# Kernel optimization log

Hardware: AMD Instinct MI355X
Metric: run time of the kernel (lower is better)

## Reference

```python
import jax, jax.numpy as jnp
import numpy as np

B, D, FH, FW, C = 8, 41, 32, 88, 64
OGFH, OGFW = 512, 1408
DX = jnp.array([0.5, 20.0, 0.5], dtype=jnp.float32)          # voxel sizes (x, y, z)
BX = jnp.array([-49.75, 0.0, -49.75], dtype=jnp.float32)    # voxel centers origin
NX = (200, 1, 200)                                           # grid dims (x, y, z)
NSEG = NX[0] * NX[1] * NX[2] * B                             # 320000 voxel-batch slots


def _frustum():
    # (D, FH, FW, 3) pixel-u, pixel-v, depth; matches create_frustum_1camera
    ds = jnp.broadcast_to(jnp.arange(4.0, 45.0, 1.0)[:, None, None], (D, FH, FW))
    xs = jnp.broadcast_to(jnp.linspace(0.0, OGFW - 1, FW)[None, None, :], (D, FH, FW))
    ys = jnp.broadcast_to(jnp.linspace(0.0, OGFH - 1, FH)[None, :, None], (D, FH, FW))
    return jnp.stack([xs, ys, ds], axis=-1).astype(jnp.float32)


def setup_inputs() -> dict:
    key = jax.random.key(0)
    k1, = jax.random.split(key, 1)
    x = jax.random.normal(k1, (B, D, FH, FW, C), dtype=jnp.float32)
    # realistic pinhole intrinsics: fx=fy=800, principal point at image center
    K = np.array([[800.0, 0.0, OGFW / 2.0],
                  [0.0, 800.0, OGFH / 2.0],
                  [0.0, 0.0, 1.0]], dtype=np.float32)
    intrins = jnp.asarray(np.broadcast_to(K, (B, 3, 3)).copy())
    post_rots = jnp.broadcast_to(jnp.eye(3, dtype=jnp.float32), (B, 3, 3)) + jnp.zeros((B, 3, 3), jnp.float32)
    post_trans = jnp.zeros((B, 3), dtype=jnp.float32)
    return {"x": x, "intrins": intrins, "post_rots": post_rots, "post_trans": post_trans}


def _forward(x, intrins, post_rots, post_trans):
    # ---- get_geometry ----
    pts = _frustum()[None] - post_trans[:, None, None, None, :]          # (B,D,FH,FW,3)
    pts = jnp.einsum('bij,bdhwj->bdhwi', jnp.linalg.inv(post_rots), pts)
    pts = jnp.concatenate([pts[..., :2] * pts[..., 2:3], pts[..., 2:3]], axis=-1)
    geom = jnp.einsum('bij,bdhwj->bdhwi', jnp.linalg.inv(intrins), pts)  # camera-frame xyz

    # ---- voxel_splat ----
    Nprime = B * D * FH * FW
    xf = x.reshape(Nprime, C)
    # torch .long() truncates toward zero -> float->int cast in jnp also truncates
    coords = ((geom - (BX - DX / 2.0)) / DX).reshape(Nprime, 3).astype(jnp.int32)
    batch_ix = jnp.repeat(jnp.arange(B, dtype=jnp.int32), Nprime // B)
    kept = ((coords[:, 0] >= 0) & (coords[:, 0] < NX[0]) &
            (coords[:, 1] >= 0) & (coords[:, 1] < NX[1]) &
            (coords[:, 2] >= 0) & (coords[:, 2] < NX[2]))
    ranks = (coords[:, 0] * (NX[1] * NX[2] * B) + coords[:, 1] * (NX[2] * B) +
             coords[:, 2] * B + batch_ix)
    ranks = jnp.where(kept, ranks, NSEG)  # dump out-of-grid points into extra segment
    # segment-sum == sort + cumsum-trick pooling (sum of features per voxel)
    pooled = jax.ops.segment_sum(xf, ranks, num_segments=NSEG + 1)[:-1]  # (NSEG, C)
    final = pooled.reshape(NX[0], NX[1], NX[2], B, C)       # rank order: (x, y, z, b)
    final = jnp.transpose(final, (3, 4, 1, 2, 0))            # (B, C, ny, nz, nx)
    # torch.cat(final.unbind(dim=2), 1) -> stack ny slices along channel dim
    out = jnp.transpose(final, (0, 2, 1, 3, 4)).reshape(B, NX[1] * C, NX[2], NX[0])
    return out


def reference(x, intrins, post_rots, post_trans):
    return _forward(x, intrins, post_rots, post_trans)
```

## Files before the change

kernel.cpp:

```cpp
#include <hip/hip_runtime.h>

#define BB 8
#define DD 41
#define FHH 32
#define FWW 88
#define CC 64
#define NXX 200
#define NXZ 200
#define PLANE (NXZ * NXX)
#define OUT_ELEMS (BB * CC * PLANE)
#define ROWP 204

__global__ __launch_bounds__(256) void lss_zero_prep(
        float* __restrict__ out,
        const float* __restrict__ intrins,
        const float* __restrict__ post_rots,
        float* __restrict__ ws) {
#pragma clang fp contract(off)
    if (blockIdx.x == 0 && threadIdx.x < BB) {
        int b = threadIdx.x;
        const float* mats[2] = { post_rots + b * 9, intrins + b * 9 };
        for (int m = 0; m < 2; ++m) {
            const float* a = mats[m];
            float* o = ws + b * 18 + m * 9;
            float c00 = a[4] * a[8] - a[5] * a[7];
            float c01 = a[5] * a[6] - a[3] * a[8];
            float c02 = a[3] * a[7] - a[4] * a[6];
            float det = a[0] * c00 + a[1] * c01 + a[2] * c02;
            o[0] = c00 / det;
            o[1] = (a[2] * a[7] - a[1] * a[8]) / det;
            o[2] = (a[1] * a[5] - a[2] * a[4]) / det;
            o[3] = c01 / det;
            o[4] = (a[0] * a[8] - a[2] * a[6]) / det;
            o[5] = (a[2] * a[3] - a[0] * a[5]) / det;
            o[6] = c02 / det;
            o[7] = (a[1] * a[6] - a[0] * a[7]) / det;
            o[8] = (a[0] * a[4] - a[1] * a[3]) / det;
        }
    }
    float4 z = make_float4(0.0f, 0.0f, 0.0f, 0.0f);
    float4* o4 = reinterpret_cast<float4*>(out);
    const int n4 = OUT_ELEMS / 4;
    for (int i = blockIdx.x * 256 + threadIdx.x; i < n4; i += gridDim.x * 256)
        o4[i] = z;
}

__global__ __launch_bounds__(512) void lss_splat(
        const float* __restrict__ x,
        const float* __restrict__ post_trans,
        const float* __restrict__ invmats,
        float* __restrict__ out) {
#pragma clang fp contract(off)
    __shared__ float    srow[CC * ROWP];
    __shared__ int      scx[FWW];
    __shared__ unsigned smask[FWW];
    __shared__ int      scz;

    int blk = blockIdx.x;
    int d = blk % DD;
    int b = blk / DD;
    int tid = threadIdx.x;

    for (int i = tid; i < CC * ROWP; i += 512) srow[i] = 0.0f;

    {
        const float stepx = 1407.0f / 87.0f;
        const float stepy = 511.0f / 31.0f;
        const float* iR = invmats + b * 18;
        const float* iK = iR + 9;
        float t0 = post_trans[b * 3 + 0];
        float t1 = post_trans[b * 3 + 1];
        float t2 = post_trans[b * 3 + 2];
        float dv = 4.0f + (float)d;

        for (int t = tid; t < FWW * FHH; t += 512) {
            int w = t >> 5;
            int h = t & 31;
            float u = (float)w * stepx;
            float v = (float)h * stepy;
            float q0 = u - t0, q1 = v - t1, q2 = dv - t2;
            float p0 = fmaf(iR[2], q2, fmaf(iR[1], q1, iR[0] * q0));
            float p1 = fmaf(iR[5], q2, fmaf(iR[4], q1, iR[3] * q0));
            float p2 = fmaf(iR[8], q2, fmaf(iR[7], q1, iR[6] * q0));
            float s0 = p0 * p2;
            float s1 = p1 * p2;
            float s2 = p2;
            float g0 = fmaf(iK[2], s2, fmaf(iK[1], s1, iK[0] * s0));
            float g1 = fmaf(iK[5], s2, fmaf(iK[4], s1, iK[3] * s0));
            float g2 = fmaf(iK[8], s2, fmaf(iK[7], s1, iK[6] * s0));
            float cxf = (g0 + 50.0f) * 2.0f;
            float cyf = (g1 + 10.0f) / 20.0f;
            float czf = (g2 + 50.0f) * 2.0f;
            int cx = (int)cxf;
            int cy = (int)cyf;
            int cz = (int)czf;
            bool kept = (cx >= 0) & (cx < NXX) & (cy == 0) & (cz >= 0) & (cz < NXZ);
            unsigned long long m = __ballot(kept);
            int lane = tid & 63;
            if (lane == 0) {
                smask[w] = (unsigned)m;
                scx[w]   = min(NXX - 1, max(0, cx));
            } else if (lane == 32) {
                smask[w] = (unsigned)(m >> 32);
                scx[w]   = min(NXX - 1, max(0, cx));
            }
            if (t == 0) scz = cz;
        }
    }
    __syncthreads();

    int wv   = tid >> 6;
    int lane = tid & 63;
    int wsub = lane >> 4;
    int cq   = lane & 15;

    for (int j = 0; j < 3; ++j) {
        int w0 = 4 * wv + 32 * j;
        if (w0 >= FWW) break;
        int w = w0 + wsub;

        unsigned m = smask[w];
        int cx = scx[w];
        const float* colp = x + (((size_t)(b * DD + d) * FHH) * FWW + w) * CC + cq * 4;

        float4 acc = make_float4(0.0f, 0.0f, 0.0f, 0.0f);
#pragma unroll
        for (int hb = 0; hb < 4; ++hb) {
            float4 vals[8];
#pragma unroll
            for (int k = 0; k < 8; ++k)
                vals[k] = *reinterpret_cast<const float4*>(
                    colp + (size_t)(hb * 8 + k) * (FWW * CC));
#pragma unroll
            for (int k = 0; k < 8; ++k) {
                bool bt = (m >> (hb * 8 + k)) & 1u;
                acc.x += bt ? vals[k].x : 0.0f;
                acc.y += bt ? vals[k].y : 0.0f;
                acc.z += bt ? vals[k].z : 0.0f;
                acc.w += bt ? vals[k].w : 0.0f;
            }
        }
        if (m) {
            atomicAdd(&srow[(cq * 4 + 0) * ROWP + cx], acc.x);
            atomicAdd(&srow[(cq * 4 + 1) * ROWP + cx], acc.y);
            atomicAdd(&srow[(cq * 4 + 2) * ROWP + cx], acc.z);
            atomicAdd(&srow[(cq * 4 + 3) * ROWP + cx], acc.w);
        }
    }
    __syncthreads();

    int cz = scz;
    if (cz >= 0 && cz < NXZ) {
        size_t outBase = ((size_t)b * CC) * PLANE + (size_t)cz * NXX;
        for (int i = tid; i < CC * NXX; i += 512) {
            int c   = i / NXX;
            int cxi = i - c * NXX;
            out[outBase + (size_t)c * PLANE + cxi] = srow[c * ROWP + cxi];
        }
    }
}

extern "C" void kernel_launch(void* const* d_in, const int* in_sizes, int n_in,
                              void* d_out, int out_size, void* d_ws, size_t ws_size,
                              hipStream_t stream) {
    const float* x          = (const float*)d_in[0];
    const float* intrins    = (const float*)d_in[1];
    const float* post_rots  = (const float*)d_in[2];
    const float* post_trans = (const float*)d_in[3];
    float* out = (float*)d_out;
    float* ws  = (float*)d_ws;

    lss_zero_prep<<<2048, 256, 0, stream>>>(out, intrins, post_rots, ws);
    lss_splat<<<BB * DD, 512, 0, stream>>>(x, post_trans, ws, out);
}
```

Before: 76.88 us.

## Split splat into per-width tiles with global atomics and selective row zeroing

The splat is re-partitioned from one block per (batch, depth) to one block per (batch, depth, 8-column group), so many more blocks can run concurrently. Per-column sums are reduced with wave shuffles and added straight to the output with global atomics, replacing the full shared-memory row buffer. Zeroing is now done per output row: a small pre-kernel clears the rows that some depth maps to, and extra blocks in the splat kernel clear only the rows no depth covers, so the full-output memset pass goes away. In exchange the output needs global atomics and every block recomputes the 3x3 inverses; correctness also depends on the covered rows being cleared before any atomics land.

```diff
diff --git a/kernel.cpp b/kernel.cpp
--- a/kernel.cpp
+++ b/kernel.cpp
@@ -8,154 +8,211 @@
 #define NXX 200
 #define NXZ 200
 #define PLANE (NXZ * NXX)
-#define OUT_ELEMS (BB * CC * PLANE)
-#define ROWP 204
-
-__global__ __launch_bounds__(256) void lss_zero_prep(
-        float* __restrict__ out,
-        const float* __restrict__ intrins,
-        const float* __restrict__ post_rots,
-        float* __restrict__ ws) {
-#pragma clang fp contract(off)
-    if (blockIdx.x == 0 && threadIdx.x < BB) {
-        int b = threadIdx.x;
-        const float* mats[2] = { post_rots + b * 9, intrins + b * 9 };
-        for (int m = 0; m < 2; ++m) {
-            const float* a = mats[m];
-            float* o = ws + b * 18 + m * 9;
-            float c00 = a[4] * a[8] - a[5] * a[7];
-            float c01 = a[5] * a[6] - a[3] * a[8];
-            float c02 = a[3] * a[7] - a[4] * a[6];
-            float det = a[0] * c00 + a[1] * c01 + a[2] * c02;
-            o[0] = c00 / det;
-            o[1] = (a[2] * a[7] - a[1] * a[8]) / det;
-            o[2] = (a[1] * a[5] - a[2] * a[4]) / det;
-            o[3] = c01 / det;
-            o[4] = (a[0] * a[8] - a[2] * a[6]) / det;
-            o[5] = (a[2] * a[3] - a[0] * a[5]) / det;
-            o[6] = c02 / det;
-            o[7] = (a[1] * a[6] - a[0] * a[7]) / det;
-            o[8] = (a[0] * a[4] - a[1] * a[3]) / det;
-        }
-    }
-    float4 z = make_float4(0.0f, 0.0f, 0.0f, 0.0f);
-    float4* o4 = reinterpret_cast<float4*>(out);
-    const int n4 = OUT_ELEMS / 4;
-    for (int i = blockIdx.x * 256 + threadIdx.x; i < n4; i += gridDim.x * 256)
-        o4[i] = z;
+#define WG 8
+#define NWG (FWW / WG)
+#define NTILE (BB * DD * NWG)
+#define NROWS (BB * NXZ)
+#define STEPX (1407.0f / 87.0f)
+#define STEPY (511.0f / 31.0f)
+
+__device__ __forceinline__ void inv3x3(const float* __restrict__ a, float* o) {
+#pragma clang fp contract(off)
+    float c00 = a[4] * a[8] - a[5] * a[7];
+    float c01 = a[5] * a[6] - a[3] * a[8];
+    float c02 = a[3] * a[7] - a[4] * a[6];
+    float det = a[0] * c00 + a[1] * c01 + a[2] * c02;
+    o[0] = c00 / det;
+    o[1] = (a[2] * a[7] - a[1] * a[8]) / det;
+    o[2] = (a[1] * a[5] - a[2] * a[4]) / det;
+    o[3] = c01 / det;
+    o[4] = (a[0] * a[8] - a[2] * a[6]) / det;
+    o[5] = (a[2] * a[3] - a[0] * a[5]) / det;
+    o[6] = c02 / det;
+    o[7] = (a[1] * a[6] - a[0] * a[7]) / det;
+    o[8] = (a[0] * a[4] - a[1] * a[3]) / det;
+}
+
+__device__ __forceinline__ int cz_of(const float* iR, const float* iK,
+                                     float t0, float t1, float t2, int d) {
+#pragma clang fp contract(off)
+    float dv = 4.0f + (float)d;
+    float q0 = 0.0f - t0, q1 = 0.0f - t1, q2 = dv - t2;
+    float p0 = fmaf(iR[2], q2, fmaf(iR[1], q1, iR[0] * q0));
+    float p1 = fmaf(iR[5], q2, fmaf(iR[4], q1, iR[3] * q0));
+    float p2 = fmaf(iR[8], q2, fmaf(iR[7], q1, iR[6] * q0));
+    float s0 = p0 * p2, s1 = p1 * p2, s2 = p2;
+    float g2 = fmaf(iK[8], s2, fmaf(iK[7], s1, iK[6] * s0));
+    float czf = (g2 + 50.0f) * 2.0f;
+    return (int)czf;
+}
+
+__global__ __launch_bounds__(256) void lss_zero_cov(
+        const float* __restrict__ intrins, const float* __restrict__ post_rots,
+        const float* __restrict__ post_trans, float* __restrict__ out) {
+#pragma clang fp contract(off)
+    __shared__ int scz;
+    int blk = blockIdx.x;
+    int d = blk % DD, b = blk / DD;
+    if (threadIdx.x == 0) {
+        float iR[9], iK[9];
+        inv3x3(post_rots + b * 9, iR);
+        inv3x3(intrins + b * 9, iK);
+        scz = cz_of(iR, iK, post_trans[b*3], post_trans[b*3+1], post_trans[b*3+2], d);
+    }
+    __syncthreads();
+    int cz = scz;
+    if (cz < 0 || cz >= NXZ) return;
+    float4 z = make_float4(0.f, 0.f, 0.f, 0.f);
+    size_t base = ((size_t)b * CC) * PLANE + (size_t)cz * NXX;
+    for (int i = threadIdx.x; i < CC * (NXX / 4); i += 256) {
+        int c = i / (NXX / 4), q = i - c * (NXX / 4);
+        *reinterpret_cast<float4*>(out + base + (size_t)c * PLANE + q * 4) = z;
+    }
 }
 
 __global__ __launch_bounds__(512) void lss_splat(
         const float* __restrict__ x,
-        const float* __restrict__ post_trans,
-        const float* __restrict__ invmats,
-        float* __restrict__ out) {
-#pragma clang fp contract(off)
-    __shared__ float    srow[CC * ROWP];
-    __shared__ int      scx[FWW];
-    __shared__ unsigned smask[FWW];
-    __shared__ int      scz;
+        const float* __restrict__ intrins, const float* __restrict__ post_rots,
+        const float* __restrict__ post_trans, float* __restrict__ out) {
+#pragma clang fp contract(off)
+    __shared__ float sInv[18];
+    __shared__ int   scx[WG];
+    __shared__ unsigned smask[WG];
+    __shared__ int   scz;
+    __shared__ float ltile[WG][CC + 1];
+    __shared__ int   sflag;
 
     int blk = blockIdx.x;
-    int d = blk % DD;
-    int b = blk / DD;
     int tid = threadIdx.x;
 
-    for (int i = tid; i < CC * ROWP; i += 512) srow[i] = 0.0f;
-
-    {
-        const float stepx = 1407.0f / 87.0f;
-        const float stepy = 511.0f / 31.0f;
-        const float* iR = invmats + b * 18;
-        const float* iK = iR + 9;
-        float t0 = post_trans[b * 3 + 0];
-        float t1 = post_trans[b * 3 + 1];
-        float t2 = post_trans[b * 3 + 2];
+    if (blk >= NTILE) {
+        int r  = blk - NTILE;
+        int b  = r / NXZ;
+        int czr = r - b * NXZ;
+        if (tid == 0) {
+            inv3x3(post_rots + b * 9, sInv);
+            inv3x3(intrins  + b * 9, sInv + 9);
+        }
+        __syncthreads();
+        if (tid < 64) {
+            bool cov = false;
+            if (tid < DD)
+                cov = (cz_of(sInv, sInv + 9, post_trans[b*3], post_trans[b*3+1],
+                             post_trans[b*3+2], tid) == czr);
+            int any = __any(cov);
+            if (tid == 0) sflag = any;
+        }
+        __syncthreads();
+        if (sflag) return;
+        float4 z = make_float4(0.f, 0.f, 0.f, 0.f);
+        size_t base = ((size_t)b * CC) * PLANE + (size_t)czr * NXX;
+        for (int i = tid; i < CC * (NXX / 4); i += 512) {
+            int c = i / (NXX / 4), q = i - c * (NXX / 4);
+            *reinterpret_cast<float4*>(out + base + (size_t)c * PLANE + q * 4) = z;
+        }
+        return;
+    }
+
+    int wg = blk % NWG;
+    int t2 = blk / NWG;
+    int d  = t2 % DD;
+    int b  = t2 / DD;
+    int w0 = wg * WG;
+
+    float t0 = post_trans[b * 3 + 0];
+    float t1 = post_trans[b * 3 + 1];
+    float t2f = post_trans[b * 3 + 2];
+
+    if (tid == 0) {
+        inv3x3(post_rots + b * 9, sInv);
+        inv3x3(intrins  + b * 9, sInv + 9);
+    }
+    __syncthreads();
+
+    if (tid < WG * FHH) {
+        int wi = tid >> 5;
+        int h  = tid & 31;
+        const float* iR = sInv;
+        const float* iK = sInv + 9;
+        float u  = (float)(w0 + wi) * STEPX;
+        float v  = (float)h * STEPY;
         float dv = 4.0f + (float)d;
-
-        for (int t = tid; t < FWW * FHH; t += 512) {
-            int w = t >> 5;
-            int h = t & 31;
-            float u = (float)w * stepx;
-            float v = (float)h * stepy;
-            float q0 = u - t0, q1 = v - t1, q2 = dv - t2;
-            float p0 = fmaf(iR[2], q2, fmaf(iR[1], q1, iR[0] * q0));
-            float p1 = fmaf(iR[5], q2, fmaf(iR[4], q1, iR[3] * q0));
-            float p2 = fmaf(iR[8], q2, fmaf(iR[7], q1, iR[6] * q0));
-            float s0 = p0 * p2;
-            float s1 = p1 * p2;
-            float s2 = p2;
-            float g0 = fmaf(iK[2], s2, fmaf(iK[1], s1, iK[0] * s0));
-            float g1 = fmaf(iK[5], s2, fmaf(iK[4], s1, iK[3] * s0));
-            float g2 = fmaf(iK[8], s2, fmaf(iK[7], s1, iK[6] * s0));
-            float cxf = (g0 + 50.0f) * 2.0f;
-            float cyf = (g1 + 10.0f) / 20.0f;
-            float czf = (g2 + 50.0f) * 2.0f;
-            int cx = (int)cxf;
-            int cy = (int)cyf;
-            int cz = (int)czf;
-            bool kept = (cx >= 0) & (cx < NXX) & (cy == 0) & (cz >= 0) & (cz < NXZ);
-            unsigned long long m = __ballot(kept);
-            int lane = tid & 63;
-            if (lane == 0) {
-                smask[w] = (unsigned)m;
-                scx[w]   = min(NXX - 1, max(0, cx));
-            } else if (lane == 32) {
-                smask[w] = (unsigned)(m >> 32);
-                scx[w]   = min(NXX - 1, max(0, cx));
-            }
-            if (t == 0) scz = cz;
-        }
+        float q0 = u - t0, q1 = v - t1, q2 = dv - t2f;
+        float p0 = fmaf(iR[2], q2, fmaf(iR[1], q1, iR[0] * q0));
+        float p1 = fmaf(iR[5], q2, fmaf(iR[4], q1, iR[3] * q0));
+        float p2 = fmaf(iR[8], q2, fmaf(iR[7], q1, iR[6] * q0));
+        float s0 = p0 * p2, s1 = p1 * p2, s2 = p2;
+        float g0 = fmaf(iK[2], s2, fmaf(iK[1], s1, iK[0] * s0));
+        float g1 = fmaf(iK[5], s2, fmaf(iK[4], s1, iK[3] * s0));
+        float g2 = fmaf(iK[8], s2, fmaf(iK[7], s1, iK[6] * s0));
+        float cxf = (g0 + 50.0f) * 2.0f;
+        float cyf = (g1 + 10.0f) / 20.0f;
+        float czf = (g2 + 50.0f) * 2.0f;
+        int cx = (int)cxf;
+        int cy = (int)cyf;
+        int cz = (int)czf;
+        bool kept = (cx >= 0) & (cx < NXX) & (cy == 0) & (cz >= 0) & (cz < NXZ);
+        unsigned long long m = __ballot(kept);
+        int lane = tid & 63;
+        if (lane == 0) {
+            smask[wi] = (unsigned)m;
+            scx[wi]   = min(NXX - 1, max(0, cx));
+        } else if (lane == 32) {
+            smask[wi] = (unsigned)(m >> 32);
+            scx[wi]   = min(NXX - 1, max(0, cx));
+        }
+        if (tid == 0)
+            scz = cz_of(iR, iK, t0, t1, t2f, d);
     }
     __syncthreads();
 
     int wv   = tid >> 6;
     int lane = tid & 63;
-    int wsub = lane >> 4;
     int cq   = lane & 15;
-
-    for (int j = 0; j < 3; ++j) {
-        int w0 = 4 * wv + 32 * j;
-        if (w0 >= FWW) break;
-        int w = w0 + wsub;
-
-        unsigned m = smask[w];
-        int cx = scx[w];
-        const float* colp = x + (((size_t)(b * DD + d) * FHH) * FWW + w) * CC + cq * 4;
-
-        float4 acc = make_float4(0.0f, 0.0f, 0.0f, 0.0f);
+    int hsub = lane >> 4;
+    int w    = w0 + wv;
+
+    const float* colp = x + (((size_t)(b * DD + d) * FHH) * FWW + w) * CC + cq * 4;
+    unsigned m = smask[wv];
+
+    float4 vals[8];
 #pragma unroll
-        for (int hb = 0; hb < 4; ++hb) {
-            float4 vals[8];
+    for (int hh = 0; hh < 8; ++hh) {
+        int h = hh * 4 + hsub;
+        vals[hh] = *reinterpret_cast<const float4*>(colp + (size_t)h * (FWW * CC));
+    }
+    float4 acc = make_float4(0.f, 0.f, 0.f, 0.f);
 #pragma unroll
-            for (int k = 0; k < 8; ++k)
-                vals[k] = *reinterpret_cast<const float4*>(
-                    colp + (size_t)(hb * 8 + k) * (FWW * CC));
+    for (int hh = 0; hh < 8; ++hh) {
+        int h = hh * 4 + hsub;
+        bool bt = (m >> h) & 1u;
+        acc.x += bt ? vals[hh].x : 0.0f;
+        acc.y += bt ? vals[hh].y : 0.0f;
+        acc.z += bt ? vals[hh].z : 0.0f;
+        acc.w += bt ? vals[hh].w : 0.0f;
+    }
 #pragma unroll
-            for (int k = 0; k < 8; ++k) {
-                bool bt = (m >> (hb * 8 + k)) & 1u;
-                acc.x += bt ? vals[k].x : 0.0f;
-                acc.y += bt ? vals[k].y : 0.0f;
-                acc.z += bt ? vals[k].z : 0.0f;
-                acc.w += bt ? vals[k].w : 0.0f;
-            }
-        }
-        if (m) {
-            atomicAdd(&srow[(cq * 4 + 0) * ROWP + cx], acc.x);
-            atomicAdd(&srow[(cq * 4 + 1) * ROWP + cx], acc.y);
-            atomicAdd(&srow[(cq * 4 + 2) * ROWP + cx], acc.z);
-            atomicAdd(&srow[(cq * 4 + 3) * ROWP + cx], acc.w);
-        }
+    for (int mm = 16; mm <= 32; mm <<= 1) {
+        acc.x += __shfl_xor(acc.x, mm, 64);
+        acc.y += __shfl_xor(acc.y, mm, 64);
+        acc.z += __shfl_xor(acc.z, mm, 64);
+        acc.w += __shfl_xor(acc.w, mm, 64);
+    }
+    if (hsub == 0) {
+        ltile[wv][cq * 4 + 0] = acc.x;
+        ltile[wv][cq * 4 + 1] = acc.y;
+        ltile[wv][cq * 4 + 2] = acc.z;
+        ltile[wv][cq * 4 + 3] = acc.w;
     }
     __syncthreads();
 
     int cz = scz;
     if (cz >= 0 && cz < NXZ) {
-        size_t outBase = ((size_t)b * CC) * PLANE + (size_t)cz * NXX;
-        for (int i = tid; i < CC * NXX; i += 512) {
-            int c   = i / NXX;
-            int cxi = i - c * NXX;
-            out[outBase + (size_t)c * PLANE + cxi] = srow[c * ROWP + cxi];
+        int ch = tid >> 3;
+        int wi = tid & 7;
+        if (smask[wi]) {
+            size_t addr = ((size_t)b * CC + ch) * PLANE + (size_t)cz * NXX + scx[wi];
+            atomicAdd(out + addr, ltile[wi][ch]);
         }
     }
 }
@@ -168,8 +225,7 @@
     const float* post_rots  = (const float*)d_in[2];
     const float* post_trans = (const float*)d_in[3];
     float* out = (float*)d_out;
-    float* ws  = (float*)d_ws;
-
-    lss_zero_prep<<<2048, 256, 0, stream>>>(out, intrins, post_rots, ws);
-    lss_splat<<<BB * DD, 512, 0, stream>>>(x, post_trans, ws, out);
-}
+
+    lss_zero_cov<<<BB * DD, 256, 0, stream>>>(intrins, post_rots, post_trans, out);
+    lss_splat<<<NTILE + NROWS, 512, 0, stream>>>(x, intrins, post_rots, post_trans, out);
+}
```

After: 80.30 us. 4.4% more time.
